# Performance work log

Measured on AMD Instinct MI355X. Metric: run time of the kernel, lower is better.

Reference implementation:

```python
import jax, jax.numpy as jnp
import numpy as np

B, L, H, F, D = 8, 2048, 1024, 256, 3  # batch, seq, d_model, adapter bottleneck, non-news domains
EPS = 1e-6  # annotated-transformer LayerNorm eps


def setup_inputs() -> dict:
    key = jax.random.key(0)
    ks = jax.random.split(key, 6)
    s1 = 1.0 / np.sqrt(H)
    s2 = 1.0 / np.sqrt(F)
    return {
        "x": jax.random.normal(ks[0], (B, L, H), jnp.float32),
        # per-domain LayerNorm params (SublayerConnection.norm)
        "ln_g": jnp.ones((D, H), jnp.float32),
        "ln_b": jnp.zeros((D, H), jnp.float32),
        # per-domain adapter FFN: Linear(H->F), ReLU, Linear(F->H)
        "W1": (jax.random.normal(ks[1], (D, F, H), jnp.float32) * s1),
        "b1": jnp.zeros((D, F), jnp.float32),
        "W2": (jax.random.normal(ks[2], (D, H, F), jnp.float32) * s2),
        "b2": jnp.zeros((D, H), jnp.float32),
        # per-domain gate Linear(2H -> 1), split into the x-half (gu) and adapter-half (gv)
        "gu": (jax.random.normal(ks[3], (D, H), jnp.float32) * s1),
        "gv": (jax.random.normal(ks[4], (D, H), jnp.float32) * s1),
        "gb": jnp.zeros((D,), jnp.float32),
    }


def reference(x, ln_g, ln_b, W1, b1, W2, b2, gu, gv, gb):
    # mix_output=True, used_domain_list=['news','book','bible','iwslt'],
    # target_domain='book' (in list -> no extra pass), dropout=eval (identity).
    mu = jnp.mean(x, axis=-1, keepdims=True)
    sd = jnp.std(x, axis=-1, keepdims=True, ddof=1)  # torch .std default (unbiased)
    xn = (x - mu) / (sd + EPS)                        # shared normalization stats
    # per-domain LayerNorm affine -> [D,B,L,H]
    h = xn[None] * ln_g[:, None, None, :] + ln_b[:, None, None, :]
    # adapter FFN (wo_residual_forward): Linear -> ReLU -> Linear
    mid = jax.nn.relu(jnp.einsum('dblh,dfh->dblf', h, W1) + b1[:, None, None, :])
    a = jnp.einsum('dblf,dhf->dblh', mid, W2) + b2[:, None, None, :]  # [D,B,L,H]
    # gate = sigmoid(Linear([x; a])) with W_gate split as [gu | gv]
    gate = jax.nn.sigmoid(
        jnp.einsum('blh,dh->dbl', x, gu)
        + jnp.einsum('dblh,dh->dbl', a, gv)
        + gb[:, None, None]
    )  # [D,B,L]
    # stacked sum includes 'news' contribution (= x), then outer residual +x:
    return 2.0 * x + jnp.sum(gate[..., None] * a, axis=0)
```

## Files before the change

kernel.cpp:

```cpp
#include <hip/hip_runtime.h>
#include <cstdint>

#define T_TOK 16384
#define H 1024
#define F 256
#define D 3
#define DF 768

typedef unsigned short u16;
typedef __attribute__((ext_vector_type(8))) short short8;
typedef __attribute__((ext_vector_type(4))) float floatx4;

__device__ __forceinline__ u16 f2bf(float f) {
  unsigned u = __float_as_uint(f);
  u += 0x7fff + ((u >> 16) & 1);
  return (u16)(u >> 16);
}
__device__ __forceinline__ float bf2f(u16 s) {
  return __uint_as_float(((unsigned)s) << 16);
}

__device__ __forceinline__ void gload_lds16(const void* g, void* l) {
  __builtin_amdgcn_global_load_lds(
      reinterpret_cast<const __attribute__((address_space(1))) void*>(
          reinterpret_cast<uintptr_t>(g)),
      reinterpret_cast<__attribute__((address_space(3))) void*>(
          reinterpret_cast<uintptr_t>(l)),
      16, 0, 0);
}

#define FENCE() asm volatile("" ::: "memory")
#define BAR1() do { FENCE(); __builtin_amdgcn_s_barrier(); \
    asm volatile("s_waitcnt lgkmcnt(0)" ::: "memory"); \
    __builtin_amdgcn_sched_barrier(0); } while (0)
#define BAR2() do { FENCE(); __builtin_amdgcn_s_barrier(); FENCE(); } while (0)
#define VMC(n) asm volatile("s_waitcnt vmcnt(" #n ")" ::: "memory")

__device__ __forceinline__ float block_reduce_256(float v, float* red, int tid) {
  #pragma unroll
  for (int o = 32; o > 0; o >>= 1) v += __shfl_xor(v, o);
  __syncthreads();
  if ((tid & 63) == 0) red[tid >> 6] = v;
  __syncthreads();
  return red[0] + red[1] + red[2] + red[3];
}


__global__ __launch_bounds__(256)
void prep_elem(const float* __restrict__ W1, const float* __restrict__ lng,
               u16* __restrict__ W1p, const float* __restrict__ W2,
               u16* __restrict__ W2r)
{
  int idx = blockIdx.x * 256 + threadIdx.x;
  int stride = gridDim.x * 256;
  for (int i = idx; i < D * F * H; i += stride) {
    int h = i & (H - 1);
    int d = i / (F * H);
    W1p[i] = f2bf(W1[i] * lng[d * H + h]);
  }
  for (int i = idx; i < H * DF; i += stride) {
    int k = i % DF;
    int hh = i / DF;
    int d = k >> 8;
    int f = k & (F - 1);
    W2r[i] = f2bf(W2[((size_t)d * H + hh) * F + f]);
  }
}

__global__ __launch_bounds__(256)
void prep_dots(const float* __restrict__ W1, const float* __restrict__ lnb,
               const float* __restrict__ b1, const float* __restrict__ W2,
               const float* __restrict__ gv, const float* __restrict__ b2,
               const float* __restrict__ gb, float* __restrict__ b1p,
               float* __restrict__ wg, float* __restrict__ cg)
{
  __shared__ float red[4];
  int d = blockIdx.x >> 8;
  int f = blockIdx.x & 255;
  int tid = threadIdx.x;
  float s1 = 0.f, s2 = 0.f, s3 = 0.f;
  for (int h = tid; h < H; h += 256) {
    float w1v = W1[((size_t)d * F + f) * H + h];
    float gvv = gv[d * H + h];
    s1 += lnb[d * H + h] * w1v;
    s2 += W2[((size_t)d * H + h) * F + f] * gvv;
    if (f == 0) s3 += b2[d * H + h] * gvv;
  }
  float S1 = block_reduce_256(s1, red, tid);
  float S2 = block_reduce_256(s2, red, tid);
  if (tid == 0) {
    b1p[d * F + f] = b1[d * F + f] + S1;
    wg[d * F + f] = S2;
  }
  if (f == 0) {
    float S3 = block_reduce_256(s3, red, tid);
    if (tid == 0) cg[d] = gb[d] + S3;
  }
}

__global__ __launch_bounds__(256)
void ln_xu_kernel(const float* __restrict__ x, const float* __restrict__ gu,
                  u16* __restrict__ xn, float* __restrict__ xu)
{
  int t = blockIdx.x;
  int tid = threadIdx.x;
  const float4 xv = *reinterpret_cast<const float4*>(x + (size_t)t * H + tid * 4);
  const float4 g0 = *reinterpret_cast<const float4*>(gu + tid * 4);
  const float4 g1 = *reinterpret_cast<const float4*>(gu + H + tid * 4);
  const float4 g2 = *reinterpret_cast<const float4*>(gu + 2 * H + tid * 4);
  float s  = xv.x + xv.y + xv.z + xv.w;
  float sq = xv.x * xv.x + xv.y * xv.y + xv.z * xv.z + xv.w * xv.w;
  float d0 = xv.x * g0.x + xv.y * g0.y + xv.z * g0.z + xv.w * g0.w;
  float d1 = xv.x * g1.x + xv.y * g1.y + xv.z * g1.z + xv.w * g1.w;
  float d2 = xv.x * g2.x + xv.y * g2.y + xv.z * g2.z + xv.w * g2.w;
  #pragma unroll
  for (int o = 32; o > 0; o >>= 1) {
    s  += __shfl_xor(s, o);  sq += __shfl_xor(sq, o);
    d0 += __shfl_xor(d0, o); d1 += __shfl_xor(d1, o); d2 += __shfl_xor(d2, o);
  }
  __shared__ float red[4][5];
  int w = tid >> 6;
  if ((tid & 63) == 0) {
    red[w][0] = s; red[w][1] = sq; red[w][2] = d0; red[w][3] = d1; red[w][4] = d2;
  }
  __syncthreads();
  float S  = red[0][0] + red[1][0] + red[2][0] + red[3][0];
  float SQ = red[0][1] + red[1][1] + red[2][1] + red[3][1];
  float mu = S * (1.0f / H);
  float var = (SQ - (float)H * mu * mu) * (1.0f / (H - 1));
  float rs = 1.0f / (sqrtf(fmaxf(var, 0.0f)) + 1e-6f);
  ushort4 o4;
  o4.x = f2bf((xv.x - mu) * rs);
  o4.y = f2bf((xv.y - mu) * rs);
  o4.z = f2bf((xv.z - mu) * rs);
  o4.w = f2bf((xv.w - mu) * rs);
  *reinterpret_cast<ushort4*>(xn + (size_t)t * H + tid * 4) = o4;
  if (tid == 0) {
    xu[t]             = red[0][2] + red[1][2] + red[2][2] + red[3][2];
    xu[T_TOK + t]     = red[0][3] + red[1][3] + red[2][3] + red[3][3];
    xu[2 * T_TOK + t] = red[0][4] + red[1][4] + red[2][4] + red[3][4];
  }
}

template <int K, int NLD, int EPI>
__global__ __launch_bounds__(512, 4)
void gemm3s(const u16* __restrict__ A, const u16* __restrict__ Bm,
            const float* __restrict__ p0,
            const float* __restrict__ p1,
            const float* __restrict__ p2,
            const float* __restrict__ p3,
            u16* __restrict__ o16,
            float* __restrict__ o32,
            int nBx)
{
  constexpr int NS = K / 32;
  constexpr int SLOT = 12288;
  extern __shared__ u16 LD[];

  const int tid = threadIdx.x, lane = tid & 63, w = tid >> 6;
  const int wm = w >> 2, wn = w & 3, lr = lane & 15, sl = lane >> 4;

  const int nwg = gridDim.x;
  const int wgs = (blockIdx.x & 7) * (nwg >> 3) + (blockIdx.x >> 3);
  const int bx = wgs % nBx, by = wgs / nBx;
  const int m0 = by * 128, n0 = bx * 256;

  const u16* Asrc = A + (size_t)m0 * K;
  const u16* Bsrc = Bm + (size_t)n0 * K;

  const int goff0 = (tid >> 2) * K + (tid & 3) * 8;
  const int goff1 = goff0 + 128 * K;
  const int w512 = w * 512;

  const int sl8 = sl * 8;
  const int aoff = (wm * 64 + lr) * 32 + sl8;
  const int boff = 4096 + (wn * 64 + lr) * 32 + sl8;

  floatx4 acc[4][4] = {};
  short8 a[4], b[4];

#define STG(P, ks) do { \
    gload_lds16(Asrc + goff0 + (ks) * 32, (P) + w512); \
    gload_lds16(Bsrc + goff0 + (ks) * 32, (P) + 4096 + w512); \
    gload_lds16(Bsrc + goff1 + (ks) * 32, (P) + 8192 + w512); \
  } while (0)
#define LDAB(P) do { const u16* sa_ = (P) + aoff; const u16* sb_ = (P) + boff; \
    _Pragma("unroll") for (int i_ = 0; i_ < 4; ++i_) { \
      a[i_] = *reinterpret_cast<const short8*>(sa_ + i_ * 512); \
      b[i_] = *reinterpret_cast<const short8*>(sb_ + i_ * 512); } } while (0)
#define MM() do { __builtin_amdgcn_s_setprio(1); \
    _Pragma("unroll") for (int mf_ = 0; mf_ < 4; ++mf_) \
      _Pragma("unroll") for (int nf_ = 0; nf_ < 4; ++nf_) \
        acc[mf_][nf_] = __builtin_amdgcn_mfma_f32_16x16x32_bf16( \
            a[mf_], b[nf_], acc[mf_][nf_], 0, 0, 0); \
    __builtin_amdgcn_s_setprio(0); } while (0)

  STG(LD, 0);
  STG(LD + SLOT, 1);
  VMC(3);
  BAR2();

  int s = 0;
  #pragma unroll 3
  for (int p = 0; p < NS - 3; ++p) {
    u16* cur = LD + s * SLOT;
    int s2 = s + 2; if (s2 >= 3) s2 -= 3;
    LDAB(cur);
    STG(LD + s2 * SLOT, p + 2);
    BAR1(); MM(); VMC(3); BAR2();
    ++s; if (s == 3) s = 0;
  }
  {
    u16* cur = LD + s * SLOT;
    int s2 = s + 2; if (s2 >= 3) s2 -= 3;
    LDAB(cur);
    STG(LD + s2 * SLOT, NS - 1);
    BAR1(); MM(); VMC(3); BAR2();
    ++s; if (s == 3) s = 0;
  }
  {
    u16* cur = LD + s * SLOT;
    LDAB(cur);
    BAR1(); MM(); VMC(0); BAR2();
    ++s; if (s == 3) s = 0;
  }
  {
    u16* cur = LD + s * SLOT;
    LDAB(cur);
    BAR1(); MM(); BAR2();
  }
  BAR2();

  if constexpr (EPI == 1) {
    float b1v[4], wgv[4];
    #pragma unroll
    for (int nf = 0; nf < 4; ++nf) {
      int col = n0 + wn * 64 + nf * 16 + lr;
      b1v[nf] = p0[col];
      wgv[nf] = p1[col];
    }
    float* red = (float*)LD;
    #pragma unroll
    for (int mf = 0; mf < 4; ++mf)
      #pragma unroll
      for (int i2 = 0; i2 < 4; ++i2) {
        float p = 0.f;
        #pragma unroll
        for (int nf = 0; nf < 4; ++nf)
          p += fmaxf(acc[mf][nf][i2] + b1v[nf], 0.f) * wgv[nf];
        p += __shfl_xor(p, 1); p += __shfl_xor(p, 2);
        p += __shfl_xor(p, 4); p += __shfl_xor(p, 8);
        if (lr == 0) red[wn * 128 + wm * 64 + mf * 16 + sl * 4 + i2] = p;
      }
    __syncthreads();
    const int d = bx;
    const float cgv = p3[d];
    #pragma unroll
    for (int mf = 0; mf < 4; ++mf)
      #pragma unroll
      for (int i2 = 0; i2 < 4; ++i2) {
        int rl = wm * 64 + mf * 16 + sl * 4 + i2;
        int r = m0 + rl;
        float logit = red[rl] + red[128 + rl] + red[256 + rl] + red[384 + rl]
                    + p2[(size_t)d * T_TOK + r] + cgv;
        float g = 1.f / (1.f + expf(-logit));
        #pragma unroll
        for (int nf = 0; nf < 4; ++nf) {
          int col = n0 + wn * 64 + nf * 16 + lr;
          float v = fmaxf(acc[mf][nf][i2] + b1v[nf], 0.f);
          o16[(size_t)r * NLD + col] = f2bf(v * g);
        }
        if (lr == 0 && wn == 0) o32[(size_t)d * T_TOK + r] = g;
      }
  } else {
    float b2v[3][4];
    #pragma unroll
    for (int dd = 0; dd < 3; ++dd)
      #pragma unroll
      for (int nf = 0; nf < 4; ++nf)
        b2v[dd][nf] = p2[dd * H + n0 + wn * 64 + nf * 16 + lr];
    #pragma unroll
    for (int mf = 0; mf < 4; ++mf)
      #pragma unroll
      for (int i2 = 0; i2 < 4; ++i2) {
        int r = m0 + wm * 64 + mf * 16 + sl * 4 + i2;
        float g0 = p1[r], g1 = p1[T_TOK + r], g2 = p1[2 * T_TOK + r];
        const float* xrow = p0 + (size_t)r * H;
        float* orow = o32 + (size_t)r * NLD;
        #pragma unroll
        for (int nf = 0; nf < 4; ++nf) {
          int col = n0 + wn * 64 + nf * 16 + lr;
          orow[col] = acc[mf][nf][i2] + 2.f * xrow[col]
                    + g0 * b2v[0][nf] + g1 * b2v[1][nf] + g2 * b2v[2][nf];
        }
      }
  }
#undef STG
#undef LDAB
#undef MM
}


extern "C" void kernel_launch(void* const* d_in, const int* in_sizes, int n_in,
                              void* d_out, int out_size, void* d_ws, size_t ws_size,
                              hipStream_t stream) {
  const float* x   = (const float*)d_in[0];
  const float* lng = (const float*)d_in[1];
  const float* lnb = (const float*)d_in[2];
  const float* W1  = (const float*)d_in[3];
  const float* b1  = (const float*)d_in[4];
  const float* W2  = (const float*)d_in[5];
  const float* b2  = (const float*)d_in[6];
  const float* gu  = (const float*)d_in[7];
  const float* gv  = (const float*)d_in[8];
  const float* gb  = (const float*)d_in[9];
  float* out = (float*)d_out;

  char* ws = (char*)d_ws;
  u16* xn   = (u16*)ws;  ws += (size_t)T_TOK * H * 2;
  u16* mid  = (u16*)ws;  ws += (size_t)T_TOK * DF * 2;
  u16* W1p  = (u16*)ws;  ws += (size_t)DF * H * 2;
  u16* W2r  = (u16*)ws;  ws += (size_t)H * DF * 2;
  float* b1p  = (float*)ws;  ws += DF * 4;
  float* wg   = (float*)ws;  ws += DF * 4;
  float* cg   = (float*)ws;  ws += 256;
  float* xu   = (float*)ws;  ws += (size_t)D * T_TOK * 4;
  float* gate = (float*)ws;  ws += (size_t)D * T_TOK * 4;
  (void)ws_size; (void)in_sizes; (void)n_in; (void)out_size;

  hipFuncSetAttribute(reinterpret_cast<const void*>(&gemm3s<1024, DF, 1>),
                      hipFuncAttributeMaxDynamicSharedMemorySize, 73728);
  hipFuncSetAttribute(reinterpret_cast<const void*>(&gemm3s<768, H, 2>),
                      hipFuncAttributeMaxDynamicSharedMemorySize, 73728);

  prep_elem<<<3072, 256, 0, stream>>>(W1, lng, W1p, W2, W2r);
  prep_dots<<<DF, 256, 0, stream>>>(W1, lnb, b1, W2, gv, b2, gb, b1p, wg, cg);
  ln_xu_kernel<<<T_TOK, 256, 0, stream>>>(x, gu, xn, xu);
  gemm3s<1024, DF, 1><<<128 * 3, 512, 73728, stream>>>(
      xn, W1p, b1p, wg, xu, cg, mid, gate, 3);
  gemm3s<768, H, 2><<<128 * 4, 512, 73728, stream>>>(
      mid, W2r, x, gate, b2, nullptr, nullptr, out, 4);
}
```

Measured before the change: 131.2 us.

## Load GEMM A operand directly to registers and swizzle B tiles in LDS

The GEMM kernel now double-buffers the A operand fragments straight from global memory into registers instead of staging them through LDS. Only the B tile goes through LDS, with an XOR swizzle on the 16-byte chunks to avoid bank conflicts. This cuts shared memory per block from 72KB to 48KB and reworks the pipeline into a two-step unrolled loop with adjusted vmcnt waits. It adds register pressure, and A rows are now fetched by each wave separately, so overlapping waves read them redundantly from global or L2.

```diff
diff --git a/kernel.cpp b/kernel.cpp
--- a/kernel.cpp
+++ b/kernel.cpp
@@ -30,10 +30,9 @@
 }
 
 #define FENCE() asm volatile("" ::: "memory")
-#define BAR1() do { FENCE(); __builtin_amdgcn_s_barrier(); \
-    asm volatile("s_waitcnt lgkmcnt(0)" ::: "memory"); \
+#define BARX() do { FENCE(); __builtin_amdgcn_s_barrier(); FENCE(); } while (0)
+#define LGKM0() do { asm volatile("s_waitcnt lgkmcnt(0)" ::: "memory"); \
     __builtin_amdgcn_sched_barrier(0); } while (0)
-#define BAR2() do { FENCE(); __builtin_amdgcn_s_barrier(); FENCE(); } while (0)
 #define VMC(n) asm volatile("s_waitcnt vmcnt(" #n ")" ::: "memory")
 
 __device__ __forceinline__ float block_reduce_256(float v, float* red, int tid) {
@@ -144,17 +143,17 @@
 
 template <int K, int NLD, int EPI>
 __global__ __launch_bounds__(512, 4)
-void gemm3s(const u16* __restrict__ A, const u16* __restrict__ Bm,
-            const float* __restrict__ p0,
-            const float* __restrict__ p1,
-            const float* __restrict__ p2,
-            const float* __restrict__ p3,
-            u16* __restrict__ o16,
-            float* __restrict__ o32,
-            int nBx)
+void gemmd(const u16* __restrict__ A, const u16* __restrict__ Bm,
+           const float* __restrict__ p0,
+           const float* __restrict__ p1,
+           const float* __restrict__ p2,
+           const float* __restrict__ p3,
+           u16* __restrict__ o16,
+           float* __restrict__ o32,
+           int nBx)
 {
-  constexpr int NS = K / 32;
-  constexpr int SLOT = 12288;
+  constexpr int NT = K / 32;
+  constexpr int SLOT = 8192;
   extern __shared__ u16 LD[];
 
   const int tid = threadIdx.x, lane = tid & 63, w = tid >> 6;
@@ -165,71 +164,89 @@
   const int bx = wgs % nBx, by = wgs / nBx;
   const int m0 = by * 128, n0 = bx * 256;
 
-  const u16* Asrc = A + (size_t)m0 * K;
+  const u16* Aptr = A + (size_t)(m0 + wm * 64 + lr) * K + sl * 8;
   const u16* Bsrc = Bm + (size_t)n0 * K;
 
-  const int goff0 = (tid >> 2) * K + (tid & 3) * 8;
-  const int goff1 = goff0 + 128 * K;
-  const int w512 = w * 512;
-
-  const int sl8 = sl * 8;
-  const int aoff = (wm * 64 + lr) * 32 + sl8;
-  const int boff = 4096 + (wn * 64 + lr) * 32 + sl8;
+  const int c0r = tid >> 2, c0s = tid & 3;
+  const int c1r = (tid + 512) >> 2, c1s = tid & 3;
+  const int key0 = (c0r ^ (c0r >> 2)) & 3;
+  const int key1 = (c1r ^ (c1r >> 2)) & 3;
+  const u16* gB0 = Bsrc + (size_t)c0r * K + ((c0s ^ key0) << 3);
+  const u16* gB1 = Bsrc + (size_t)c1r * K + ((c1s ^ key1) << 3);
+  const int ldst0 = w * 512;
+  const int ldst1 = 4096 + w * 512;
+
+  const int rkey = (lr ^ (lr >> 2)) & 3;
+  const int boff = (wn * 64 + lr) * 32 + ((sl ^ rkey) << 3);
 
   floatx4 acc[4][4] = {};
-  short8 a[4], b[4];
-
-#define STG(P, ks) do { \
-    gload_lds16(Asrc + goff0 + (ks) * 32, (P) + w512); \
-    gload_lds16(Bsrc + goff0 + (ks) * 32, (P) + 4096 + w512); \
-    gload_lds16(Bsrc + goff1 + (ks) * 32, (P) + 8192 + w512); \
+  short8 aA[4], aB[4], b[4];
+
+#define STGB(SP, T_) do { \
+    gload_lds16(gB0 + (T_) * 32, (SP) + ldst0); \
+    gload_lds16(gB1 + (T_) * 32, (SP) + ldst1); \
   } while (0)
-#define LDAB(P) do { const u16* sa_ = (P) + aoff; const u16* sb_ = (P) + boff; \
-    _Pragma("unroll") for (int i_ = 0; i_ < 4; ++i_) { \
-      a[i_] = *reinterpret_cast<const short8*>(sa_ + i_ * 512); \
-      b[i_] = *reinterpret_cast<const short8*>(sb_ + i_ * 512); } } while (0)
-#define MM() do { __builtin_amdgcn_s_setprio(1); \
+#define PREFA(AR, T_) do { \
+    _Pragma("unroll") for (int mf_ = 0; mf_ < 4; ++mf_) \
+      AR[mf_] = *reinterpret_cast<const short8*>( \
+          Aptr + (size_t)mf_ * 16 * K + (T_) * 32); } while (0)
+#define LDB(SP) do { const u16* sb_ = (SP) + boff; \
+    _Pragma("unroll") for (int nf_ = 0; nf_ < 4; ++nf_) \
+      b[nf_] = *reinterpret_cast<const short8*>(sb_ + nf_ * 512); } while (0)
+#define MMX(AR) do { __builtin_amdgcn_s_setprio(1); \
     _Pragma("unroll") for (int mf_ = 0; mf_ < 4; ++mf_) \
       _Pragma("unroll") for (int nf_ = 0; nf_ < 4; ++nf_) \
         acc[mf_][nf_] = __builtin_amdgcn_mfma_f32_16x16x32_bf16( \
-            a[mf_], b[nf_], acc[mf_][nf_], 0, 0, 0); \
+            AR[mf_], b[nf_], acc[mf_][nf_], 0, 0, 0); \
     __builtin_amdgcn_s_setprio(0); } while (0)
 
-  STG(LD, 0);
-  STG(LD + SLOT, 1);
-  VMC(3);
-  BAR2();
-
-  int s = 0;
-  #pragma unroll 3
-  for (int p = 0; p < NS - 3; ++p) {
-    u16* cur = LD + s * SLOT;
+  PREFA(aA, 0);
+  STGB(LD, 0);
+  STGB(LD + SLOT, 1);
+  STGB(LD + 2 * SLOT, 2);
+  PREFA(aB, 1);
+  VMC(8); BARX();
+  LDB(LD); LGKM0(); MMX(aA); BARX();
+
+  int s = 1;
+  #pragma unroll 1
+  for (int i = 0; i < (NT - 4) / 2; ++i) {
+    const int t = 2 * i + 1;
+    {
+      int s2 = s + 2; if (s2 >= 3) s2 -= 3;
+      STGB(LD + s2 * SLOT, t + 2);
+      PREFA(aA, t + 1);
+      VMC(6); BARX();
+      LDB(LD + s * SLOT); LGKM0(); MMX(aB); BARX();
+      ++s; if (s == 3) s = 0;
+    }
+    {
+      int s2 = s + 2; if (s2 >= 3) s2 -= 3;
+      STGB(LD + s2 * SLOT, t + 3);
+      PREFA(aB, t + 2);
+      VMC(6); BARX();
+      LDB(LD + s * SLOT); LGKM0(); MMX(aA); BARX();
+      ++s; if (s == 3) s = 0;
+    }
+  }
+  {
     int s2 = s + 2; if (s2 >= 3) s2 -= 3;
-    LDAB(cur);
-    STG(LD + s2 * SLOT, p + 2);
-    BAR1(); MM(); VMC(3); BAR2();
+    STGB(LD + s2 * SLOT, NT - 1);
+    PREFA(aA, NT - 2);
+    VMC(6); BARX();
+    LDB(LD + s * SLOT); LGKM0(); MMX(aB); BARX();
     ++s; if (s == 3) s = 0;
   }
   {
-    u16* cur = LD + s * SLOT;
-    int s2 = s + 2; if (s2 >= 3) s2 -= 3;
-    LDAB(cur);
-    STG(LD + s2 * SLOT, NS - 1);
-    BAR1(); MM(); VMC(3); BAR2();
+    PREFA(aB, NT - 1);
+    VMC(4); BARX();
+    LDB(LD + s * SLOT); LGKM0(); MMX(aA); BARX();
     ++s; if (s == 3) s = 0;
   }
   {
-    u16* cur = LD + s * SLOT;
-    LDAB(cur);
-    BAR1(); MM(); VMC(0); BAR2();
-    ++s; if (s == 3) s = 0;
-  }
-  {
-    u16* cur = LD + s * SLOT;
-    LDAB(cur);
-    BAR1(); MM(); BAR2();
-  }
-  BAR2();
+    VMC(0); BARX();
+    LDB(LD + s * SLOT); LGKM0(); MMX(aB); BARX();
+  }
 
   if constexpr (EPI == 1) {
     float b1v[4], wgv[4];
@@ -295,9 +312,10 @@
         }
       }
   }
-#undef STG
-#undef LDAB
-#undef MM
+#undef STGB
+#undef PREFA
+#undef LDB
+#undef MMX
 }
 
 
@@ -328,16 +346,16 @@
   float* gate = (float*)ws;  ws += (size_t)D * T_TOK * 4;
   (void)ws_size; (void)in_sizes; (void)n_in; (void)out_size;
 
-  hipFuncSetAttribute(reinterpret_cast<const void*>(&gemm3s<1024, DF, 1>),
-                      hipFuncAttributeMaxDynamicSharedMemorySize, 73728);
-  hipFuncSetAttribute(reinterpret_cast<const void*>(&gemm3s<768, H, 2>),
-                      hipFuncAttributeMaxDynamicSharedMemorySize, 73728);
+  hipFuncSetAttribute(reinterpret_cast<const void*>(&gemmd<1024, DF, 1>),
+                      hipFuncAttributeMaxDynamicSharedMemorySize, 49152);
+  hipFuncSetAttribute(reinterpret_cast<const void*>(&gemmd<768, H, 2>),
+                      hipFuncAttributeMaxDynamicSharedMemorySize, 49152);
 
   prep_elem<<<3072, 256, 0, stream>>>(W1, lng, W1p, W2, W2r);
   prep_dots<<<DF, 256, 0, stream>>>(W1, lnb, b1, W2, gv, b2, gb, b1p, wg, cg);
   ln_xu_kernel<<<T_TOK, 256, 0, stream>>>(x, gu, xn, xu);
-  gemm3s<1024, DF, 1><<<128 * 3, 512, 73728, stream>>>(
+  gemmd<1024, DF, 1><<<128 * 3, 512, 49152, stream>>>(
       xn, W1p, b1p, wg, xu, cg, mid, gate, 3);
-  gemm3s<768, H, 2><<<128 * 4, 512, 73728, stream>>>(
+  gemmd<768, H, 2><<<128 * 4, 512, 49152, stream>>>(
       mid, W2r, x, gate, b2, nullptr, nullptr, out, 4);
 }
```

After: 212.7 us. +62.1%, slower.

## Replace triple-buffered GEMM pipeline with swizzled double-buffered loop and column-major tile order

Applied to the files above, without the earlier changes.

Both adapter GEMMs move from a 3-slot LDS ring with hand-placed waitcnt and barrier macros to a simpler double-buffered loop that uses __syncthreads, and shared memory per block shrinks. LDS tiles now use an XOR swizzle on the 16-byte chunk index, applied on the global-to-LDS load and on the fragment reads, to cut bank conflicts. Tile traversal changes so that consecutive workgroups walk down M for a fixed N column, which changes L2 reuse of the weight tiles. The shallower pipeline and the coarse barriers risk exposing more global-load latency than the previous hand-scheduled version.

```diff
diff --git a/kernel.cpp b/kernel.cpp
--- a/kernel.cpp
+++ b/kernel.cpp
@@ -28,13 +28,6 @@
           reinterpret_cast<uintptr_t>(l)),
       16, 0, 0);
 }
-
-#define FENCE() asm volatile("" ::: "memory")
-#define BAR1() do { FENCE(); __builtin_amdgcn_s_barrier(); \
-    asm volatile("s_waitcnt lgkmcnt(0)" ::: "memory"); \
-    __builtin_amdgcn_sched_barrier(0); } while (0)
-#define BAR2() do { FENCE(); __builtin_amdgcn_s_barrier(); FENCE(); } while (0)
-#define VMC(n) asm volatile("s_waitcnt vmcnt(" #n ")" ::: "memory")
 
 __device__ __forceinline__ float block_reduce_256(float v, float* red, int tid) {
   #pragma unroll
@@ -144,17 +137,17 @@
 
 template <int K, int NLD, int EPI>
 __global__ __launch_bounds__(512, 4)
-void gemm3s(const u16* __restrict__ A, const u16* __restrict__ Bm,
+void gemm2p(const u16* __restrict__ A, const u16* __restrict__ Bm,
             const float* __restrict__ p0,
             const float* __restrict__ p1,
             const float* __restrict__ p2,
             const float* __restrict__ p3,
             u16* __restrict__ o16,
             float* __restrict__ o32,
-            int nBx)
+            int nBy)
 {
-  constexpr int NS = K / 32;
-  constexpr int SLOT = 12288;
+  constexpr int NT = K / 32;
+  constexpr int BUF = 12288;
   extern __shared__ u16 LD[];
 
   const int tid = threadIdx.x, lane = tid & 63, w = tid >> 6;
@@ -162,74 +155,58 @@
 
   const int nwg = gridDim.x;
   const int wgs = (blockIdx.x & 7) * (nwg >> 3) + (blockIdx.x >> 3);
-  const int bx = wgs % nBx, by = wgs / nBx;
+  const int by = wgs % nBy, bx = wgs / nBy;
   const int m0 = by * 128, n0 = bx * 256;
 
   const u16* Asrc = A + (size_t)m0 * K;
   const u16* Bsrc = Bm + (size_t)n0 * K;
 
-  const int goff0 = (tid >> 2) * K + (tid & 3) * 8;
-  const int goff1 = goff0 + 128 * K;
-  const int w512 = w * 512;
-
-  const int sl8 = sl * 8;
-  const int aoff = (wm * 64 + lr) * 32 + sl8;
-  const int boff = 4096 + (wn * 64 + lr) * 32 + sl8;
+  const int sc = (tid & 3) ^ ((tid >> 3) & 3);
+  const int srcA  = (tid >> 2) * K + sc * 8;
+  const int srcB1 = srcA + 128 * K;
+  const int dstA  = w * 512;
+  const int dstB0 = 4096 + w * 512;
+  const int dstB1 = 8192 + w * 512;
+
+  const int key = (lr >> 1) & 3;
+  const int rsl = (sl ^ key) << 3;
+  const int aoff = (wm * 64 + lr) * 32 + rsl;
+  const int boff = 4096 + (wn * 64 + lr) * 32 + rsl;
 
   floatx4 acc[4][4] = {};
   short8 a[4], b[4];
 
-#define STG(P, ks) do { \
-    gload_lds16(Asrc + goff0 + (ks) * 32, (P) + w512); \
-    gload_lds16(Bsrc + goff0 + (ks) * 32, (P) + 4096 + w512); \
-    gload_lds16(Bsrc + goff1 + (ks) * 32, (P) + 8192 + w512); \
+#define STG(BP, T_) do { int kb_ = (T_) * 32; \
+    gload_lds16(Asrc + srcA + kb_, (BP) + dstA); \
+    gload_lds16(Bsrc + srcA + kb_, (BP) + dstB0); \
+    gload_lds16(Bsrc + srcB1 + kb_, (BP) + dstB1); \
   } while (0)
-#define LDAB(P) do { const u16* sa_ = (P) + aoff; const u16* sb_ = (P) + boff; \
+#define LDAB(BP) do { \
+    const u16* sa_ = (BP) + aoff; const u16* sb_ = (BP) + boff; \
     _Pragma("unroll") for (int i_ = 0; i_ < 4; ++i_) { \
       a[i_] = *reinterpret_cast<const short8*>(sa_ + i_ * 512); \
       b[i_] = *reinterpret_cast<const short8*>(sb_ + i_ * 512); } } while (0)
-#define MM() do { __builtin_amdgcn_s_setprio(1); \
+#define MMX() do { \
     _Pragma("unroll") for (int mf_ = 0; mf_ < 4; ++mf_) \
       _Pragma("unroll") for (int nf_ = 0; nf_ < 4; ++nf_) \
         acc[mf_][nf_] = __builtin_amdgcn_mfma_f32_16x16x32_bf16( \
-            a[mf_], b[nf_], acc[mf_][nf_], 0, 0, 0); \
-    __builtin_amdgcn_s_setprio(0); } while (0)
+            a[mf_], b[nf_], acc[mf_][nf_], 0, 0, 0); } while (0)
 
   STG(LD, 0);
-  STG(LD + SLOT, 1);
-  VMC(3);
-  BAR2();
-
-  int s = 0;
-  #pragma unroll 3
-  for (int p = 0; p < NS - 3; ++p) {
-    u16* cur = LD + s * SLOT;
-    int s2 = s + 2; if (s2 >= 3) s2 -= 3;
+  __syncthreads();
+
+  #pragma unroll 1
+  for (int t = 0; t < NT - 1; ++t) {
+    u16* cur = LD + (t & 1) * BUF;
+    u16* nxt = LD + ((t + 1) & 1) * BUF;
+    STG(nxt, t + 1);
     LDAB(cur);
-    STG(LD + s2 * SLOT, p + 2);
-    BAR1(); MM(); VMC(3); BAR2();
-    ++s; if (s == 3) s = 0;
-  }
-  {
-    u16* cur = LD + s * SLOT;
-    int s2 = s + 2; if (s2 >= 3) s2 -= 3;
-    LDAB(cur);
-    STG(LD + s2 * SLOT, NS - 1);
-    BAR1(); MM(); VMC(3); BAR2();
-    ++s; if (s == 3) s = 0;
-  }
-  {
-    u16* cur = LD + s * SLOT;
-    LDAB(cur);
-    BAR1(); MM(); VMC(0); BAR2();
-    ++s; if (s == 3) s = 0;
-  }
-  {
-    u16* cur = LD + s * SLOT;
-    LDAB(cur);
-    BAR1(); MM(); BAR2();
-  }
-  BAR2();
+    MMX();
+    __syncthreads();
+  }
+  LDAB(LD + ((NT - 1) & 1) * BUF);
+  MMX();
+  __syncthreads();
 
   if constexpr (EPI == 1) {
     float b1v[4], wgv[4];
@@ -297,7 +274,7 @@
   }
 #undef STG
 #undef LDAB
-#undef MM
+#undef MMX
 }
 
 
@@ -328,16 +305,16 @@
   float* gate = (float*)ws;  ws += (size_t)D * T_TOK * 4;
   (void)ws_size; (void)in_sizes; (void)n_in; (void)out_size;
 
-  hipFuncSetAttribute(reinterpret_cast<const void*>(&gemm3s<1024, DF, 1>),
-                      hipFuncAttributeMaxDynamicSharedMemorySize, 73728);
-  hipFuncSetAttribute(reinterpret_cast<const void*>(&gemm3s<768, H, 2>),
-                      hipFuncAttributeMaxDynamicSharedMemorySize, 73728);
+  hipFuncSetAttribute(reinterpret_cast<const void*>(&gemm2p<1024, DF, 1>),
+                      hipFuncAttributeMaxDynamicSharedMemorySize, 49152);
+  hipFuncSetAttribute(reinterpret_cast<const void*>(&gemm2p<768, H, 2>),
+                      hipFuncAttributeMaxDynamicSharedMemorySize, 49152);
 
   prep_elem<<<3072, 256, 0, stream>>>(W1, lng, W1p, W2, W2r);
   prep_dots<<<DF, 256, 0, stream>>>(W1, lnb, b1, W2, gv, b2, gb, b1p, wg, cg);
   ln_xu_kernel<<<T_TOK, 256, 0, stream>>>(x, gu, xn, xu);
-  gemm3s<1024, DF, 1><<<128 * 3, 512, 73728, stream>>>(
-      xn, W1p, b1p, wg, xu, cg, mid, gate, 3);
-  gemm3s<768, H, 2><<<128 * 4, 512, 73728, stream>>>(
-      mid, W2r, x, gate, b2, nullptr, nullptr, out, 4);
-}
+  gemm2p<1024, DF, 1><<<128 * 3, 512, 49152, stream>>>(
+      xn, W1p, b1p, wg, xu, cg, mid, gate, 128);
+  gemm2p<768, H, 2><<<128 * 4, 512, 49152, stream>>>(
+      mid, W2r, x, gate, b2, nullptr, nullptr, out, 128);
+}
```

After: 132.6 us. Within noise of the previous version (+1.1%).
